# Kernel optimization log

Hardware: AMD Instinct MI355X
Metric: run time of the kernel (lower is better)

Reference implementation:

```python
import jax, jax.numpy as jnp
import numpy as np

B, S, E, H, F = 32, 512, 1024, 8, 8192
D = E // H  # head_dim = 128


def setup_inputs() -> dict:
    key = jax.random.key(0)
    ks = jax.random.split(key, 6)
    w = 0.02  # init scale
    return {
        "x": jax.random.normal(ks[0], (B, S, E), dtype=jnp.float32),
        "Wq": jax.random.normal(ks[1], (E, E), dtype=jnp.float32) * w,
        "bq": jnp.zeros((E,), dtype=jnp.float32),
        "Wk": jax.random.normal(ks[2], (E, E), dtype=jnp.float32) * w,
        "bk": jnp.zeros((E,), dtype=jnp.float32),
        "Wv": jax.random.normal(ks[3], (E, E), dtype=jnp.float32) * w,
        "bv": jnp.zeros((E,), dtype=jnp.float32),
        "W1": jax.random.normal(ks[4], (E, F), dtype=jnp.float32) * w,
        "b1": jnp.zeros((F,), dtype=jnp.float32),
        "W2": jax.random.normal(ks[5], (F, E), dtype=jnp.float32) * w,
        "b2": jnp.zeros((E,), dtype=jnp.float32),
    }


def reference(x, Wq, bq, Wk, bk, Wv, bv, W1, b1, W2, b2):
    b, s, e = x.shape
    h, d = H, e // H
    # headed projections: [b, h, s, d]
    q = (x @ Wq + bq).reshape(b, s, h, d).transpose(0, 2, 1, 3)
    k = (x @ Wk + bk).reshape(b, s, h, d).transpose(0, 2, 1, 3)
    v = (x @ Wv + bv).reshape(b, s, h, d).transpose(0, 2, 1, 3)
    # NOTE: original applies NO 1/sqrt(d) scaling
    scores = jnp.einsum("bhqd,bhkd->bhqk", q, k)
    attn = jax.nn.softmax(scores, axis=-1)
    o = jnp.einsum("bhqk,bhkd->bhqd", attn, v)
    o = o.transpose(0, 2, 1, 3).reshape(b, s, e)  # concat heads
    hid = jax.nn.gelu(o @ W1 + b1, approximate=False)  # nn.GELU default = exact erf
    return hid @ W2 + b2
```

## Files before the change

### kernel.cpp

```cpp
#include <hip/hip_runtime.h>
#include <hip/hip_bf16.h>
#include <math.h>

typedef __attribute__((ext_vector_type(8))) short bf16x8;
typedef __attribute__((ext_vector_type(4))) float f32x4;
typedef __hip_bfloat16 bf16;

__device__ __forceinline__ void gload_lds16(const void* g, void* l) {
  __builtin_amdgcn_global_load_lds((const __attribute__((address_space(1))) void*)g,
                                   (__attribute__((address_space(3))) void*)l,
                                   16, 0, 0);
}

__device__ __forceinline__ float gelu_erf(float x) {
  return 0.5f * x * (1.0f + erff(x * 0.70710678118654752f));
}

__global__ __launch_bounds__(256) void k_cvt_bf16(const float* __restrict__ in,
                                                  bf16* __restrict__ out, int n4) {
  int i = blockIdx.x * 256 + threadIdx.x;
  const int stride = gridDim.x * 256;
  for (; i < n4; i += stride) {
    float4 v = reinterpret_cast<const float4*>(in)[i];
    bf16* o = out + (size_t)i * 4;
    o[0] = __float2bfloat16(v.x);
    o[1] = __float2bfloat16(v.y);
    o[2] = __float2bfloat16(v.z);
    o[3] = __float2bfloat16(v.w);
  }
}

__global__ __launch_bounds__(256) void k_concat_bias(const float* __restrict__ bq,
                                                     const float* __restrict__ bk,
                                                     const float* __restrict__ bv,
                                                     float* __restrict__ cbias) {
  const int i = blockIdx.x * 256 + threadIdx.x;
  const float v = (i < 1024) ? bq[i] : (i < 2048) ? bk[i - 1024] : bv[i - 2048];
  cbias[i] = v;
}

__global__ __launch_bounds__(256) void k_transpose_w(const float* __restrict__ in,
                                                     bf16* __restrict__ out,
                                                     int R, int C) {
  __shared__ float tile[32][33];
  const int c0 = blockIdx.x * 32, r0 = blockIdx.y * 32;
  const int tx = threadIdx.x & 31, ty = threadIdx.x >> 5;
  for (int i = 0; i < 32; i += 8)
    tile[ty + i][tx] = in[(size_t)(r0 + ty + i) * C + c0 + tx];
  __syncthreads();
  for (int i = 0; i < 32; i += 8)
    out[(size_t)(c0 + ty + i) * R + r0 + tx] = __float2bfloat16(tile[tx][ty + i]);
}

__global__ __launch_bounds__(256) void k_transpose_v(const bf16* __restrict__ Vb,
                                                     bf16* __restrict__ Vt) {
  __shared__ bf16 tile[32][34];
  const int bh = blockIdx.z;
  const int b = bh >> 3, h = bh & 7;
  const int s0 = blockIdx.x * 32, d0 = blockIdx.y * 32;
  const int tx = threadIdx.x & 31, ty = threadIdx.x >> 5;
  for (int i = 0; i < 32; i += 8)
    tile[ty + i][tx] = Vb[((size_t)b * 512 + s0 + ty + i) * 1024 + h * 128 + d0 + tx];
  __syncthreads();
  for (int i = 0; i < 32; i += 8)
    Vt[((size_t)bh * 128 + d0 + ty + i) * 512 + s0 + tx] = tile[tx][ty + i];
}

template <int EPI, bool ACC>
__global__ __launch_bounds__(512, 2) void k_gemm256(
    const bf16* __restrict__ A, const bf16* __restrict__ Bt,
    const float* __restrict__ bias, void* __restrict__ Cout,
    int K, int lda, int ldb, int ldc) {
  __shared__ __attribute__((aligned(16))) char lds[131072];
  const int t = threadIdx.x, w = t >> 6, l = t & 63;
  const int gx = gridDim.x, nwg = gx * gridDim.y;
  int bid = blockIdx.y * gx + blockIdx.x;
  bid = (bid & 7) * (nwg >> 3) + (bid >> 3);
  const int bm = bid / gx, bn = bid % gx;
  const int wm = w >> 2, wn = w & 3;
  const int lq = l >> 4, lr = l & 15;

  const char* Ab = (const char*)(A + (size_t)(bm * 256) * lda);
  const char* Bb = (const char*)(Bt + (size_t)(bn * 256) * ldb);
  const int r0 = t >> 3, s0x = ((t & 7) ^ (r0 & 7)) << 4;
  const int r1 = (t + 512) >> 3, s1x = (((t + 512) & 7) ^ (r1 & 7)) << 4;
  const size_t la = (size_t)lda * 2, lb = (size_t)ldb * 2;
  const char* pA00 = Ab + (size_t)((r0 >> 6) * 128 + (r0 & 63)) * la + s0x;
  const char* pA10 = Ab + (size_t)((r1 >> 6) * 128 + (r1 & 63)) * la + s1x;
  const char* pA01 = Ab + (size_t)((r0 >> 6) * 128 + 64 + (r0 & 63)) * la + s0x;
  const char* pA11 = Ab + (size_t)((r1 >> 6) * 128 + 64 + (r1 & 63)) * la + s1x;
  const char* pB00 = Bb + (size_t)((r0 >> 5) * 64 + (r0 & 31)) * lb + s0x;
  const char* pB10 = Bb + (size_t)((r1 >> 5) * 64 + (r1 & 31)) * lb + s1x;
  const char* pB01 = Bb + (size_t)((r0 >> 5) * 64 + 32 + (r0 & 31)) * lb + s0x;
  const char* pB11 = Bb + (size_t)((r1 >> 5) * 64 + 32 + (r1 & 31)) * lb + s1x;

  const int swzb = (lq ^ (lr & 7)) << 4;
  const int aoff = wm * 8192 + lr * 128;
  const int boff = 32768 + wn * 4096 + lr * 128;

  f32x4 acc[8][4];
#pragma unroll
  for (int m = 0; m < 8; ++m)
#pragma unroll
    for (int n = 0; n < 4; ++n) acc[m][n] = (f32x4){0.f, 0.f, 0.f, 0.f};

#define ISSUE_A0(S) { gload_lds16(pA00, (S) + w * 1024); gload_lds16(pA10, (S) + 8192 + w * 1024); pA00 += 128; pA10 += 128; }
#define ISSUE_A1(S) { gload_lds16(pA01, (S) + 16384 + w * 1024); gload_lds16(pA11, (S) + 16384 + 8192 + w * 1024); pA01 += 128; pA11 += 128; }
#define ISSUE_B0(S) { gload_lds16(pB00, (S) + 32768 + w * 1024); gload_lds16(pB10, (S) + 32768 + 8192 + w * 1024); pB00 += 128; pB10 += 128; }
#define ISSUE_B1(S) { gload_lds16(pB01, (S) + 49152 + w * 1024); gload_lds16(pB11, (S) + 49152 + 8192 + w * 1024); pB01 += 128; pB11 += 128; }

  bf16x8 aF[4][2], bF01[2][2], bF23[2][2];
#define READ_A03(C) { _Pragma("unroll") for (int fr = 0; fr < 4; ++fr) _Pragma("unroll") for (int kk = 0; kk < 2; ++kk) aF[fr][kk] = *(const bf16x8*)((C) + aoff + fr * 2048 + (swzb ^ (kk << 6))); }
#define READ_A47(C) { _Pragma("unroll") for (int fr = 0; fr < 4; ++fr) _Pragma("unroll") for (int kk = 0; kk < 2; ++kk) aF[fr][kk] = *(const bf16x8*)((C) + 16384 + aoff + fr * 2048 + (swzb ^ (kk << 6))); }
#define READ_B01(C) { _Pragma("unroll") for (int fc = 0; fc < 2; ++fc) _Pragma("unroll") for (int kk = 0; kk < 2; ++kk) bF01[fc][kk] = *(const bf16x8*)((C) + boff + fc * 2048 + (swzb ^ (kk << 6))); }
#define READ_B23(C) { _Pragma("unroll") for (int fc = 0; fc < 2; ++fc) _Pragma("unroll") for (int kk = 0; kk < 2; ++kk) bF23[fc][kk] = *(const bf16x8*)((C) + 16384 + boff + fc * 2048 + (swzb ^ (kk << 6))); }

#define MFMA_Q(ACCR, BFR)                                               \
  { __builtin_amdgcn_s_setprio(1);                                      \
    _Pragma("unroll") for (int fr = 0; fr < 4; ++fr)                    \
      _Pragma("unroll") for (int fc = 0; fc < 2; ++fc)                  \
        _Pragma("unroll") for (int kk = 0; kk < 2; ++kk)                \
          acc[ACCR + fr][fc + ((&BFR == &bF23) ? 2 : 0)] =              \
              __builtin_amdgcn_mfma_f32_16x16x32_bf16(aF[fr][kk], BFR[fc][kk], acc[ACCR + fr][fc + ((&BFR == &bF23) ? 2 : 0)], 0, 0, 0); \
    __builtin_amdgcn_s_setprio(0); }

#define CLOBBER asm volatile("" ::: "memory")
#define BAR __builtin_amdgcn_s_barrier()

  ISSUE_A0(lds); ISSUE_B0(lds); ISSUE_B1(lds); ISSUE_A1(lds);
  asm volatile("s_waitcnt vmcnt(4)" ::: "memory");
  BAR; CLOBBER;

  const int NT = K >> 6;
  for (int kt = 0; kt < NT; ++kt) {
    char* cur = lds + (kt & 1) * 65536;
    char* nxt = lds + ((kt & 1) ^ 1) * 65536;
    const bool pre = (kt + 1 < NT);

    READ_A03(cur); READ_B01(cur);
    if (pre) { ISSUE_A0(nxt);
               asm volatile("s_waitcnt vmcnt(4)" ::: "memory"); }
    else     { asm volatile("s_waitcnt vmcnt(2)" ::: "memory"); }
    BAR; CLOBBER;
    MFMA_Q(0, bF01)
    BAR; CLOBBER;

    READ_B23(cur);
    if (pre) { ISSUE_B0(nxt);
               asm volatile("s_waitcnt vmcnt(4)" ::: "memory"); }
    else     { asm volatile("s_waitcnt vmcnt(0)" ::: "memory"); }
    BAR; CLOBBER;
    MFMA_Q(0, bF23)
    BAR; CLOBBER;

    READ_A47(cur);
    if (pre) ISSUE_B1(nxt);
    CLOBBER;
    BAR; CLOBBER;
    MFMA_Q(4, bF01)
    BAR; CLOBBER;

    if (pre) { ISSUE_A1(nxt);
               asm volatile("s_waitcnt vmcnt(4)" ::: "memory"); }
    else     { CLOBBER; }
    BAR; CLOBBER;
    MFMA_Q(4, bF23)
    BAR; CLOBBER;
  }
#undef ISSUE_A0
#undef ISSUE_A1
#undef ISSUE_B0
#undef ISSUE_B1
#undef READ_A03
#undef READ_A47
#undef READ_B01
#undef READ_B23
#undef MFMA_Q
#undef CLOBBER
#undef BAR

  const int rowb = bm * 256 + wm * 128;
  const int colb = bn * 256 + wn * 64;
#pragma unroll
  for (int fr = 0; fr < 8; ++fr) {
#pragma unroll
    for (int fc = 0; fc < 4; ++fc) {
      const int col = colb + fc * 16 + lr;
      const float bv = bias ? bias[col] : 0.0f;
#pragma unroll
      for (int i = 0; i < 4; ++i) {
        const int row = rowb + fr * 16 + lq * 4 + i;
        float v = acc[fr][fc][i] + bv;
        if (EPI == 1) v = gelu_erf(v);
        if (EPI <= 1) {
          ((bf16*)Cout)[(size_t)row * ldc + col] = __float2bfloat16(v);
        } else if (EPI == 3) {
          bf16* Cq = (bf16*)Cout + (size_t)(colb >> 10) * 16777216ull;
          Cq[(size_t)row * 1024 + (col & 1023)] = __float2bfloat16(v);
        } else {
          float* Cf = (float*)Cout;
          const size_t idx = (size_t)row * ldc + col;
          if (ACC) v += Cf[idx];
          Cf[idx] = v;
        }
      }
    }
  }
}

__global__ __launch_bounds__(512, 1) void k_attn(const bf16* __restrict__ Qg,
                                                 const bf16* __restrict__ Kg,
                                                 const bf16* __restrict__ Vt,
                                                 bf16* __restrict__ Og) {
  __shared__ __attribute__((aligned(16))) char lds[131072];
  int bid = blockIdx.x;
  bid = (bid & 7) * 128 + (bid >> 3);
  const int bh = bid >> 2, q0 = (bid & 3) * 128;
  const int b = bh >> 3, h = bh & 7;
  const int t = threadIdx.x, w = t >> 6, l = t & 63;
  const int lq = l >> 4, lr = l & 15;
  const int wm = w >> 2, wn = w & 3;

  const int sr = t >> 4;
  const int ss = (t & 15) ^ (sr & 15);
  {
    const bf16* ks = Kg + ((size_t)b * 512 + sr) * 1024 + h * 128 + ss * 8;
#pragma unroll
    for (int j = 0; j < 16; ++j)
      gload_lds16(ks + (size_t)j * 32 * 1024, lds + j * 8192 + w * 1024);
  }

  bf16x8 qf[4][4];
  {
    const bf16* qb = Qg + ((size_t)b * 512 + q0 + wm * 64 + lr) * 1024 + h * 128 + lq * 8;
#pragma unroll
    for (int fr = 0; fr < 4; ++fr)
#pragma unroll
      for (int d0 = 0; d0 < 4; ++d0)
        qf[fr][d0] = *(const bf16x8*)(qb + (size_t)(fr * 16) * 1024 + d0 * 32);
  }

  asm volatile("s_waitcnt vmcnt(0)" ::: "memory");
  __builtin_amdgcn_s_barrier();
  asm volatile("" ::: "memory");

  f32x4 accS[4][8];
#pragma unroll
  for (int fr = 0; fr < 4; ++fr)
#pragma unroll
    for (int fc = 0; fc < 8; ++fc) accS[fr][fc] = (f32x4){0.f, 0.f, 0.f, 0.f};

  __builtin_amdgcn_s_setprio(1);
#pragma unroll
  for (int fc = 0; fc < 8; ++fc) {
    bf16x8 kf[4];
#pragma unroll
    for (int d0 = 0; d0 < 4; ++d0)
      kf[d0] = *(const bf16x8*)(lds + (wn * 128 + fc * 16 + lr) * 256 +
                                (((d0 * 4 + lq) ^ lr) << 4));
#pragma unroll
    for (int d0 = 0; d0 < 4; ++d0)
#pragma unroll
      for (int fr = 0; fr < 4; ++fr)
        accS[fr][fc] = __builtin_amdgcn_mfma_f32_16x16x32_bf16(qf[fr][d0], kf[d0], accS[fr][fc], 0, 0, 0);
  }
  __builtin_amdgcn_s_setprio(0);

  __builtin_amdgcn_s_barrier();
  asm volatile("" ::: "memory");

  const bf16* vs = Vt + ((size_t)bh * 128 + sr) * 512 + ss * 8;
#define IVC(kc, slot)                                                         \
  {                                                                           \
    _Pragma("unroll") for (int j = 0; j < 4; ++j)                             \
        gload_lds16(vs + (size_t)j * 32 * 512 + (kc) * 128,                   \
                    lds + (slot) * 32768 + j * 8192 + w * 1024);              \
  }
  IVC(0, 0)
  IVC(1, 1)

  float* redm = (float*)(lds + 98304);
  float* reds = (float*)(lds + 100352);
  float fm[4][4];
#pragma unroll
  for (int fr = 0; fr < 4; ++fr)
#pragma unroll
    for (int i = 0; i < 4; ++i) {
      float m = accS[fr][0][i];
#pragma unroll
      for (int fc = 1; fc < 8; ++fc) m = fmaxf(m, accS[fr][fc][i]);
      m = fmaxf(m, __shfl_xor(m, 1));
      m = fmaxf(m, __shfl_xor(m, 2));
      m = fmaxf(m, __shfl_xor(m, 4));
      m = fmaxf(m, __shfl_xor(m, 8));
      if (lr == 0) redm[wn * 128 + wm * 64 + fr * 16 + lq * 4 + i] = m;
    }
  asm volatile("s_waitcnt lgkmcnt(0)" ::: "memory");
  __builtin_amdgcn_s_barrier();
  asm volatile("" ::: "memory");
#pragma unroll
  for (int fr = 0; fr < 4; ++fr)
#pragma unroll
    for (int i = 0; i < 4; ++i) {
      const int row = wm * 64 + fr * 16 + lq * 4 + i;
      fm[fr][i] = fmaxf(fmaxf(redm[row], redm[128 + row]),
                        fmaxf(redm[256 + row], redm[384 + row]));
    }

  f32x4 oacc[4][2];
#pragma unroll
  for (int fr = 0; fr < 4; ++fr)
#pragma unroll
    for (int fc = 0; fc < 2; ++fc) oacc[fr][fc] = (f32x4){0.f, 0.f, 0.f, 0.f};
  float s4[4][4];
#pragma unroll
  for (int fr = 0; fr < 4; ++fr)
#pragma unroll
    for (int i = 0; i < 4; ++i) s4[fr][i] = 0.f;

#define EXPWRITE(kc)                                                           \
  if (wn == (kc)) {                                                            \
    _Pragma("unroll") for (int fr = 0; fr < 4; ++fr)                           \
      _Pragma("unroll") for (int i = 0; i < 4; ++i) {                          \
        const int row = wm * 64 + fr * 16 + lq * 4 + i;                        \
        const int rx = lq * 4 + i;                                             \
        _Pragma("unroll") for (int fc = 0; fc < 8; ++fc) {                     \
          const float e = __expf(accS[fr][fc][i] - fm[fr][i]);                 \
          s4[fr][i] += e;                                                      \
          *(unsigned short*)(lds + 65536 + row * 256 +                         \
                             (((fc * 2 + (lr >> 3)) ^ rx) << 4) + (lr & 7) * 2) = \
              __bfloat16_as_ushort(__float2bfloat16(e));                       \
        }                                                                      \
      }                                                                        \
  }

#define PVMFMA(kc)                                                             \
  {                                                                            \
    const char* Vb = lds + ((kc) & 1) * 32768;                                 \
    __builtin_amdgcn_s_setprio(1);                                             \
    _Pragma("unroll") for (int kk = 0; kk < 4; ++kk) {                         \
      bf16x8 pa[4], vb[2];                                                     \
      _Pragma("unroll") for (int fr = 0; fr < 4; ++fr)                         \
          pa[fr] = *(const bf16x8*)(lds + 65536 + (wm * 64 + fr * 16 + lr) * 256 + \
                                    (((kk * 4 + lq) ^ lr) << 4));              \
      _Pragma("unroll") for (int fc = 0; fc < 2; ++fc)                         \
          vb[fc] = *(const bf16x8*)(Vb + (wn * 32 + fc * 16 + lr) * 256 +      \
                                    (((kk * 4 + lq) ^ lr) << 4));              \
      _Pragma("unroll") for (int fr = 0; fr < 4; ++fr)                         \
        _Pragma("unroll") for (int fc = 0; fc < 2; ++fc)                       \
          oacc[fr][fc] = __builtin_amdgcn_mfma_f32_16x16x32_bf16(pa[fr], vb[fc], oacc[fr][fc], 0, 0, 0); \
    }                                                                          \
    __builtin_amdgcn_s_setprio(0);                                             \
  }

  EXPWRITE(0)
  asm volatile("s_waitcnt lgkmcnt(0)" ::: "memory");
  asm volatile("s_waitcnt vmcnt(4)" ::: "memory");
  __builtin_amdgcn_s_barrier();
  asm volatile("" ::: "memory");
  PVMFMA(0)
  __builtin_amdgcn_s_barrier();
  asm volatile("" ::: "memory");
  IVC(2, 0)
  EXPWRITE(1)
  asm volatile("s_waitcnt lgkmcnt(0)" ::: "memory");
  asm volatile("s_waitcnt vmcnt(4)" ::: "memory");
  __builtin_amdgcn_s_barrier();
  asm volatile("" ::: "memory");
  PVMFMA(1)
  __builtin_amdgcn_s_barrier();
  asm volatile("" ::: "memory");
  IVC(3, 1)
  EXPWRITE(2)
  asm volatile("s_waitcnt lgkmcnt(0)" ::: "memory");
  asm volatile("s_waitcnt vmcnt(4)" ::: "memory");
  __builtin_amdgcn_s_barrier();
  asm volatile("" ::: "memory");
  PVMFMA(2)
  __builtin_amdgcn_s_barrier();
  asm volatile("" ::: "memory");
  EXPWRITE(3)
  asm volatile("s_waitcnt lgkmcnt(0)" ::: "memory");
  asm volatile("s_waitcnt vmcnt(0)" ::: "memory");
  __builtin_amdgcn_s_barrier();
  asm volatile("" ::: "memory");
  PVMFMA(3)
#undef IVC
#undef EXPWRITE
#undef PVMFMA

#pragma unroll
  for (int fr = 0; fr < 4; ++fr)
#pragma unroll
    for (int i = 0; i < 4; ++i) {
      float s = s4[fr][i];
      s += __shfl_xor(s, 1);
      s += __shfl_xor(s, 2);
      s += __shfl_xor(s, 4);
      s += __shfl_xor(s, 8);
      if (lr == 0) reds[wn * 128 + wm * 64 + fr * 16 + lq * 4 + i] = s;
    }
  asm volatile("s_waitcnt lgkmcnt(0)" ::: "memory");
  __builtin_amdgcn_s_barrier();
  asm volatile("" ::: "memory");

#pragma unroll
  for (int fr = 0; fr < 4; ++fr)
#pragma unroll
    for (int i = 0; i < 4; ++i) {
      const int row = wm * 64 + fr * 16 + lq * 4 + i;
      const float rs = (reds[row] + reds[128 + row]) + (reds[256 + row] + reds[384 + row]);
#pragma unroll
      for (int fc = 0; fc < 2; ++fc) {
        const int col = wn * 32 + fc * 16 + lr;
        Og[((size_t)b * 512 + q0 + row) * 1024 + h * 128 + col] =
            __float2bfloat16(oacc[fr][fc][i] / rs);
      }
    }
}

extern "C" void kernel_launch(void* const* d_in, const int* in_sizes, int n_in,
                              void* d_out, int out_size, void* d_ws, size_t ws_size,
                              hipStream_t stream) {
  (void)in_sizes; (void)n_in; (void)out_size; (void)ws_size;
  const float* x  = (const float*)d_in[0];
  const float* Wq = (const float*)d_in[1];
  const float* bq = (const float*)d_in[2];
  const float* Wk = (const float*)d_in[3];
  const float* bk = (const float*)d_in[4];
  const float* Wv = (const float*)d_in[5];
  const float* bv = (const float*)d_in[6];
  const float* W1 = (const float*)d_in[7];
  const float* b1 = (const float*)d_in[8];
  const float* W2 = (const float*)d_in[9];
  const float* b2 = (const float*)d_in[10];
  float* out = (float*)d_out;
  char* ws = (char*)d_ws;
  constexpr size_t MB = 1ull << 20;

  bf16* XB  = (bf16*)(ws + 0);
  bf16* WQT = (bf16*)(ws + 32 * MB);
  bf16* WKT = (bf16*)(ws + 34 * MB);
  bf16* WVT = (bf16*)(ws + 36 * MB);
  bf16* QB  = (bf16*)(ws + 38 * MB);
  bf16* KB  = (bf16*)(ws + 70 * MB);
  bf16* VB  = (bf16*)(ws + 102 * MB);
  bf16* VT  = (bf16*)(ws + 134 * MB);
  bf16* OB  = (bf16*)(ws + 166 * MB);
  bf16* W1T = (bf16*)(ws + 0);
  bf16* W2T = (bf16*)(ws + 16 * MB);
  bf16* HC  = (bf16*)(ws + 38 * MB);
  float* CB = (float*)(ws + 166 * MB);

  k_cvt_bf16<<<2048, 256, 0, stream>>>(x, XB, (16384 * 1024) / 4);
  k_concat_bias<<<12, 256, 0, stream>>>(bq, bk, bv, CB);
  k_transpose_w<<<dim3(32, 32), 256, 0, stream>>>(Wq, WQT, 1024, 1024);
  k_transpose_w<<<dim3(32, 32), 256, 0, stream>>>(Wk, WKT, 1024, 1024);
  k_transpose_w<<<dim3(32, 32), 256, 0, stream>>>(Wv, WVT, 1024, 1024);

  k_gemm256<3, false><<<dim3(12, 64), 512, 0, stream>>>(XB, WQT, CB, QB, 1024, 1024, 1024, 1024);

  k_transpose_w<<<dim3(256, 32), 256, 0, stream>>>(W1, W1T, 1024, 8192);
  k_transpose_w<<<dim3(32, 256), 256, 0, stream>>>(W2, W2T, 8192, 1024);

  k_transpose_v<<<dim3(16, 4, 256), 256, 0, stream>>>(VB, VT);
  k_attn<<<1024, 512, 0, stream>>>(QB, KB, VT, OB);

  for (int chk = 0; chk < 2; ++chk) {
    k_gemm256<1, false><<<dim3(16, 64), 512, 0, stream>>>(
        OB, W1T + (size_t)chk * 4096 * 1024, b1 + chk * 4096, HC, 1024, 1024, 1024, 4096);
    if (chk == 0)
      k_gemm256<2, false><<<dim3(4, 64), 512, 0, stream>>>(
          HC, W2T + chk * 4096, b2, out, 4096, 4096, 8192, 1024);
    else
      k_gemm256<2, true><<<dim3(4, 64), 512, 0, stream>>>(
          HC, W2T + chk * 4096, nullptr, out, 4096, 4096, 8192, 1024);
  }
}
```

Baseline: 927.4 us.

## Replace 256x256 GEMM with 128x256 tile, BK=32, simple double-buffered loop

Swaps the 512-thread 256x256 GEMM kernel, which used a K-step of 64 and a four-phase interleaved schedule, for a 256-thread kernel with a 128x256 tile and a K-step of 32. The new kernel uses a plain double-buffered loop: one stage load, a wait, a barrier, then one MFMA burst. LDS drops from 128KB to 48KB so more workgroups can fit per CU, and the grids double in row blocks. In exchange it loses the finer load/compute interleaving, and the smaller K-step means more barriers per unit of work. It also fixes the QKV epilogue's output-buffer selection to use the per-column index.

```diff
diff --git a/kernel.cpp b/kernel.cpp
--- a/kernel.cpp
+++ b/kernel.cpp
@@ -67,124 +67,92 @@
 }
 
 template <int EPI, bool ACC>
-__global__ __launch_bounds__(512, 2) void k_gemm256(
+__global__ __launch_bounds__(256, 2) void k_gemm128x256(
     const bf16* __restrict__ A, const bf16* __restrict__ Bt,
     const float* __restrict__ bias, void* __restrict__ Cout,
     int K, int lda, int ldb, int ldc) {
-  __shared__ __attribute__((aligned(16))) char lds[131072];
+  __shared__ __attribute__((aligned(16))) char lds[49152];
   const int t = threadIdx.x, w = t >> 6, l = t & 63;
   const int gx = gridDim.x, nwg = gx * gridDim.y;
   int bid = blockIdx.y * gx + blockIdx.x;
   bid = (bid & 7) * (nwg >> 3) + (bid >> 3);
   const int bm = bid / gx, bn = bid % gx;
-  const int wm = w >> 2, wn = w & 3;
+  const int wm = w >> 1, wn = w & 1;
   const int lq = l >> 4, lr = l & 15;
 
-  const char* Ab = (const char*)(A + (size_t)(bm * 256) * lda);
+  const int srw = w * 16 + (l >> 2);
+  const int scb = (((l & 3) ^ ((l >> 3) & 3)) << 4);
+  const size_t la = (size_t)lda * 2, lb = (size_t)ldb * 2;
+  const char* Ab = (const char*)(A + (size_t)(bm * 128) * lda);
   const char* Bb = (const char*)(Bt + (size_t)(bn * 256) * ldb);
-  const int r0 = t >> 3, s0x = ((t & 7) ^ (r0 & 7)) << 4;
-  const int r1 = (t + 512) >> 3, s1x = (((t + 512) & 7) ^ (r1 & 7)) << 4;
-  const size_t la = (size_t)lda * 2, lb = (size_t)ldb * 2;
-  const char* pA00 = Ab + (size_t)((r0 >> 6) * 128 + (r0 & 63)) * la + s0x;
-  const char* pA10 = Ab + (size_t)((r1 >> 6) * 128 + (r1 & 63)) * la + s1x;
-  const char* pA01 = Ab + (size_t)((r0 >> 6) * 128 + 64 + (r0 & 63)) * la + s0x;
-  const char* pA11 = Ab + (size_t)((r1 >> 6) * 128 + 64 + (r1 & 63)) * la + s1x;
-  const char* pB00 = Bb + (size_t)((r0 >> 5) * 64 + (r0 & 31)) * lb + s0x;
-  const char* pB10 = Bb + (size_t)((r1 >> 5) * 64 + (r1 & 31)) * lb + s1x;
-  const char* pB01 = Bb + (size_t)((r0 >> 5) * 64 + 32 + (r0 & 31)) * lb + s0x;
-  const char* pB11 = Bb + (size_t)((r1 >> 5) * 64 + 32 + (r1 & 31)) * lb + s1x;
-
-  const int swzb = (lq ^ (lr & 7)) << 4;
-  const int aoff = wm * 8192 + lr * 128;
-  const int boff = 32768 + wn * 4096 + lr * 128;
-
-  f32x4 acc[8][4];
-#pragma unroll
-  for (int m = 0; m < 8; ++m)
-#pragma unroll
-    for (int n = 0; n < 4; ++n) acc[m][n] = (f32x4){0.f, 0.f, 0.f, 0.f};
-
-#define ISSUE_A0(S) { gload_lds16(pA00, (S) + w * 1024); gload_lds16(pA10, (S) + 8192 + w * 1024); pA00 += 128; pA10 += 128; }
-#define ISSUE_A1(S) { gload_lds16(pA01, (S) + 16384 + w * 1024); gload_lds16(pA11, (S) + 16384 + 8192 + w * 1024); pA01 += 128; pA11 += 128; }
-#define ISSUE_B0(S) { gload_lds16(pB00, (S) + 32768 + w * 1024); gload_lds16(pB10, (S) + 32768 + 8192 + w * 1024); pB00 += 128; pB10 += 128; }
-#define ISSUE_B1(S) { gload_lds16(pB01, (S) + 49152 + w * 1024); gload_lds16(pB11, (S) + 49152 + 8192 + w * 1024); pB01 += 128; pB11 += 128; }
-
-  bf16x8 aF[4][2], bF01[2][2], bF23[2][2];
-#define READ_A03(C) { _Pragma("unroll") for (int fr = 0; fr < 4; ++fr) _Pragma("unroll") for (int kk = 0; kk < 2; ++kk) aF[fr][kk] = *(const bf16x8*)((C) + aoff + fr * 2048 + (swzb ^ (kk << 6))); }
-#define READ_A47(C) { _Pragma("unroll") for (int fr = 0; fr < 4; ++fr) _Pragma("unroll") for (int kk = 0; kk < 2; ++kk) aF[fr][kk] = *(const bf16x8*)((C) + 16384 + aoff + fr * 2048 + (swzb ^ (kk << 6))); }
-#define READ_B01(C) { _Pragma("unroll") for (int fc = 0; fc < 2; ++fc) _Pragma("unroll") for (int kk = 0; kk < 2; ++kk) bF01[fc][kk] = *(const bf16x8*)((C) + boff + fc * 2048 + (swzb ^ (kk << 6))); }
-#define READ_B23(C) { _Pragma("unroll") for (int fc = 0; fc < 2; ++fc) _Pragma("unroll") for (int kk = 0; kk < 2; ++kk) bF23[fc][kk] = *(const bf16x8*)((C) + 16384 + boff + fc * 2048 + (swzb ^ (kk << 6))); }
-
-#define MFMA_Q(ACCR, BFR)                                               \
-  { __builtin_amdgcn_s_setprio(1);                                      \
-    _Pragma("unroll") for (int fr = 0; fr < 4; ++fr)                    \
-      _Pragma("unroll") for (int fc = 0; fc < 2; ++fc)                  \
-        _Pragma("unroll") for (int kk = 0; kk < 2; ++kk)                \
-          acc[ACCR + fr][fc + ((&BFR == &bF23) ? 2 : 0)] =              \
-              __builtin_amdgcn_mfma_f32_16x16x32_bf16(aF[fr][kk], BFR[fc][kk], acc[ACCR + fr][fc + ((&BFR == &bF23) ? 2 : 0)], 0, 0, 0); \
-    __builtin_amdgcn_s_setprio(0); }
-
-#define CLOBBER asm volatile("" ::: "memory")
-#define BAR __builtin_amdgcn_s_barrier()
-
-  ISSUE_A0(lds); ISSUE_B0(lds); ISSUE_B1(lds); ISSUE_A1(lds);
-  asm volatile("s_waitcnt vmcnt(4)" ::: "memory");
-  BAR; CLOBBER;
-
-  const int NT = K >> 6;
+  const char* pA0 = Ab + (size_t)(srw) * la + scb;
+  const char* pA1 = Ab + (size_t)(64 + srw) * la + scb;
+  const char* pB0 = Bb + (size_t)(srw) * lb + scb;
+  const char* pB1 = Bb + (size_t)(64 + srw) * lb + scb;
+  const char* pB2 = Bb + (size_t)(128 + srw) * lb + scb;
+  const char* pB3 = Bb + (size_t)(192 + srw) * lb + scb;
+
+  const int swz = (lq ^ ((lr >> 1) & 3)) << 4;
+  const int aoff = (wm * 64 + lr) * 64 + swz;
+  const int boff = 8192 + (wn * 128 + lr) * 64 + swz;
+
+  f32x4 acc[4][8];
+#pragma unroll
+  for (int m = 0; m < 4; ++m)
+#pragma unroll
+    for (int n = 0; n < 8; ++n) acc[m][n] = (f32x4){0.f, 0.f, 0.f, 0.f};
+
+#define STAGE(slot)                                                       \
+  {                                                                       \
+    char* dst = lds + (slot) * 24576 + w * 1024;                          \
+    gload_lds16(pA0, dst);                                                \
+    gload_lds16(pA1, dst + 4096);                                         \
+    gload_lds16(pB0, dst + 8192);                                         \
+    gload_lds16(pB1, dst + 12288);                                        \
+    gload_lds16(pB2, dst + 16384);                                        \
+    gload_lds16(pB3, dst + 20480);                                        \
+    pA0 += 64; pA1 += 64; pB0 += 64; pB1 += 64; pB2 += 64; pB3 += 64;     \
+  }
+
+  const int NT = K >> 5;
+  STAGE(0)
+
   for (int kt = 0; kt < NT; ++kt) {
-    char* cur = lds + (kt & 1) * 65536;
-    char* nxt = lds + ((kt & 1) ^ 1) * 65536;
-    const bool pre = (kt + 1 < NT);
-
-    READ_A03(cur); READ_B01(cur);
-    if (pre) { ISSUE_A0(nxt);
-               asm volatile("s_waitcnt vmcnt(4)" ::: "memory"); }
-    else     { asm volatile("s_waitcnt vmcnt(2)" ::: "memory"); }
-    BAR; CLOBBER;
-    MFMA_Q(0, bF01)
-    BAR; CLOBBER;
-
-    READ_B23(cur);
-    if (pre) { ISSUE_B0(nxt);
-               asm volatile("s_waitcnt vmcnt(4)" ::: "memory"); }
-    else     { asm volatile("s_waitcnt vmcnt(0)" ::: "memory"); }
-    BAR; CLOBBER;
-    MFMA_Q(0, bF23)
-    BAR; CLOBBER;
-
-    READ_A47(cur);
-    if (pre) ISSUE_B1(nxt);
-    CLOBBER;
-    BAR; CLOBBER;
-    MFMA_Q(4, bF01)
-    BAR; CLOBBER;
-
-    if (pre) { ISSUE_A1(nxt);
-               asm volatile("s_waitcnt vmcnt(4)" ::: "memory"); }
-    else     { CLOBBER; }
-    BAR; CLOBBER;
-    MFMA_Q(4, bF23)
-    BAR; CLOBBER;
-  }
-#undef ISSUE_A0
-#undef ISSUE_A1
-#undef ISSUE_B0
-#undef ISSUE_B1
-#undef READ_A03
-#undef READ_A47
-#undef READ_B01
-#undef READ_B23
-#undef MFMA_Q
-#undef CLOBBER
-#undef BAR
-
-  const int rowb = bm * 256 + wm * 128;
-  const int colb = bn * 256 + wn * 64;
-#pragma unroll
-  for (int fr = 0; fr < 8; ++fr) {
-#pragma unroll
-    for (int fc = 0; fc < 4; ++fc) {
+    if (kt + 1 < NT) {
+      STAGE((kt + 1) & 1)
+      asm volatile("s_waitcnt vmcnt(6)" ::: "memory");
+    } else {
+      asm volatile("s_waitcnt vmcnt(0)" ::: "memory");
+    }
+    __builtin_amdgcn_s_barrier();
+    asm volatile("" ::: "memory");
+
+    const char* base = lds + (kt & 1) * 24576;
+    bf16x8 aF[4], bF[8];
+#pragma unroll
+    for (int fr = 0; fr < 4; ++fr)
+      aF[fr] = *(const bf16x8*)(base + aoff + fr * 1024);
+#pragma unroll
+    for (int fc = 0; fc < 8; ++fc)
+      bF[fc] = *(const bf16x8*)(base + boff + fc * 1024);
+    __builtin_amdgcn_s_setprio(1);
+#pragma unroll
+    for (int fr = 0; fr < 4; ++fr)
+#pragma unroll
+      for (int fc = 0; fc < 8; ++fc)
+        acc[fr][fc] = __builtin_amdgcn_mfma_f32_16x16x32_bf16(aF[fr], bF[fc], acc[fr][fc], 0, 0, 0);
+    __builtin_amdgcn_s_setprio(0);
+    __builtin_amdgcn_s_barrier();
+    asm volatile("" ::: "memory");
+  }
+#undef STAGE
+
+  const int rowb = bm * 128 + wm * 64;
+  const int colb = bn * 256 + wn * 128;
+#pragma unroll
+  for (int fr = 0; fr < 4; ++fr) {
+#pragma unroll
+    for (int fc = 0; fc < 8; ++fc) {
       const int col = colb + fc * 16 + lr;
       const float bv = bias ? bias[col] : 0.0f;
 #pragma unroll
@@ -195,7 +163,7 @@
         if (EPI <= 1) {
           ((bf16*)Cout)[(size_t)row * ldc + col] = __float2bfloat16(v);
         } else if (EPI == 3) {
-          bf16* Cq = (bf16*)Cout + (size_t)(colb >> 10) * 16777216ull;
+          bf16* Cq = (bf16*)Cout + (size_t)(col >> 10) * 16777216ull;
           Cq[(size_t)row * 1024 + (col & 1023)] = __float2bfloat16(v);
         } else {
           float* Cf = (float*)Cout;
@@ -458,7 +426,7 @@
   k_transpose_w<<<dim3(32, 32), 256, 0, stream>>>(Wk, WKT, 1024, 1024);
   k_transpose_w<<<dim3(32, 32), 256, 0, stream>>>(Wv, WVT, 1024, 1024);
 
-  k_gemm256<3, false><<<dim3(12, 64), 512, 0, stream>>>(XB, WQT, CB, QB, 1024, 1024, 1024, 1024);
+  k_gemm128x256<3, false><<<dim3(12, 128), 256, 0, stream>>>(XB, WQT, CB, QB, 1024, 1024, 1024, 1024);
 
   k_transpose_w<<<dim3(256, 32), 256, 0, stream>>>(W1, W1T, 1024, 8192);
   k_transpose_w<<<dim3(32, 256), 256, 0, stream>>>(W2, W2T, 8192, 1024);
@@ -467,13 +435,13 @@
   k_attn<<<1024, 512, 0, stream>>>(QB, KB, VT, OB);
 
   for (int chk = 0; chk < 2; ++chk) {
-    k_gemm256<1, false><<<dim3(16, 64), 512, 0, stream>>>(
+    k_gemm128x256<1, false><<<dim3(16, 128), 256, 0, stream>>>(
         OB, W1T + (size_t)chk * 4096 * 1024, b1 + chk * 4096, HC, 1024, 1024, 1024, 4096);
     if (chk == 0)
-      k_gemm256<2, false><<<dim3(4, 64), 512, 0, stream>>>(
+      k_gemm128x256<2, false><<<dim3(4, 128), 256, 0, stream>>>(
           HC, W2T + chk * 4096, b2, out, 4096, 4096, 8192, 1024);
     else
-      k_gemm256<2, true><<<dim3(4, 64), 512, 0, stream>>>(
+      k_gemm128x256<2, true><<<dim3(4, 128), 256, 0, stream>>>(
           HC, W2T + chk * 4096, nullptr, out, 4096, 4096, 8192, 1024);
   }
 }
```

Result: slower. 983.7 us (+6.1%).

## Deepen GEMM global-to-LDS prefetch to two k-tiles ahead

Applied to the files above, without the earlier changes.

The prologue now loads the first two k-tiles into both LDS buffers, and the main loop refills the current buffer with tile kt+2 once each quarter has been read. The vmcnt waits are retuned to match the deeper queue of in-flight loads. The aim is to hide more global memory latency behind the MFMA work. The cost is a more fragile wait and barrier schedule, since the buffer being refilled is the one that was just read.

```diff
diff --git a/kernel.cpp b/kernel.cpp
--- a/kernel.cpp
+++ b/kernel.cpp
@@ -126,44 +126,44 @@
 
 #define CLOBBER asm volatile("" ::: "memory")
 #define BAR __builtin_amdgcn_s_barrier()
+#define VMW(n) asm volatile("s_waitcnt vmcnt(" #n ")" ::: "memory")
 
   ISSUE_A0(lds); ISSUE_B0(lds); ISSUE_B1(lds); ISSUE_A1(lds);
-  asm volatile("s_waitcnt vmcnt(4)" ::: "memory");
-  BAR; CLOBBER;
+  {
+    char* s1 = lds + 65536;
+    ISSUE_A0(s1); ISSUE_B0(s1); ISSUE_B1(s1); ISSUE_A1(s1);
+  }
 
   const int NT = K >> 6;
   for (int kt = 0; kt < NT; ++kt) {
     char* cur = lds + (kt & 1) * 65536;
-    char* nxt = lds + ((kt & 1) ^ 1) * 65536;
-    const bool pre = (kt + 1 < NT);
-
+    const bool pre1 = (kt + 1 < NT);
+    const bool pre2 = (kt + 2 < NT);
+
+    if (pre1) { VMW(12); } else { VMW(4); }
+    BAR; CLOBBER;
     READ_A03(cur); READ_B01(cur);
-    if (pre) { ISSUE_A0(nxt);
-               asm volatile("s_waitcnt vmcnt(4)" ::: "memory"); }
-    else     { asm volatile("s_waitcnt vmcnt(2)" ::: "memory"); }
-    BAR; CLOBBER;
     MFMA_Q(0, bF01)
     BAR; CLOBBER;
 
+    if (pre1) { VMW(10); } else { VMW(2); }
+    BAR; CLOBBER;
     READ_B23(cur);
-    if (pre) { ISSUE_B0(nxt);
-               asm volatile("s_waitcnt vmcnt(4)" ::: "memory"); }
-    else     { asm volatile("s_waitcnt vmcnt(0)" ::: "memory"); }
-    BAR; CLOBBER;
+    if (pre2) { ISSUE_A0(cur); ISSUE_B0(cur); }
     MFMA_Q(0, bF23)
     BAR; CLOBBER;
 
+    if (pre2)      { VMW(12); }
+    else if (pre1) { VMW(8); }
+    else           { VMW(0); }
+    BAR; CLOBBER;
     READ_A47(cur);
-    if (pre) ISSUE_B1(nxt);
+    if (pre2) ISSUE_B1(cur);
+    MFMA_Q(4, bF01)
+    BAR; CLOBBER;
+
+    if (pre2) ISSUE_A1(cur);
     CLOBBER;
-    BAR; CLOBBER;
-    MFMA_Q(4, bF01)
-    BAR; CLOBBER;
-
-    if (pre) { ISSUE_A1(nxt);
-               asm volatile("s_waitcnt vmcnt(4)" ::: "memory"); }
-    else     { CLOBBER; }
-    BAR; CLOBBER;
     MFMA_Q(4, bF23)
     BAR; CLOBBER;
   }
@@ -178,6 +178,7 @@
 #undef MFMA_Q
 #undef CLOBBER
 #undef BAR
+#undef VMW
 
   const int rowb = bm * 256 + wm * 128;
   const int colb = bn * 256 + wn * 64;
```

After: 910.7 us. No clear change (-1.8%).
